# Optimization experiments

Measured on AMD Instinct MI355X. Metric: run time of the kernel, lower is better.

Reference implementation:

```python
import jax, jax.numpy as jnp
import numpy as np

N = 2048          # num agents / graph nodes
D = 128           # n_actor == n_map
ALPHA = 0.2       # GAT leakyrelu alpha
NEG = -1e9
X_IDX = [4, 9, 14, 19]   # actors_inter_cat time indices per LSTM step
E_IDX = [0, 4, 9, 14]    # graph_adjs time indices per LSTM step


def setup_inputs() -> dict:
    key = jax.random.key(0)
    ks = jax.random.split(key, 10)
    xavier = lambda k, shape: jax.random.uniform(
        k, shape, jnp.float32, -1.0, 1.0) * 1.414 * np.sqrt(6.0 / (shape[-2] + shape[-1]))
    actors_inter_cat = jax.random.normal(ks[0], (N, 20, D), jnp.float32)
    graph_adjs = jax.random.randint(ks[1], (N, 20, N), 0, 2, jnp.int32)
    # 4 GAT_SRF gates (forget, input, input_cell, output), stacked on leading axis
    Wg = xavier(ks[2], (4, 2 * D, D))          # gate projection W: in=2*D, out=D
    ag = xavier(ks[3], (4, 2 * D))             # attention vector a (2*out_features,)
    W = xavier(ks[4], (D, D))                  # GAT cell output projection
    b = xavier(ks[5], (1, D))
    h0 = xavier(ks[6], (1, D))
    conv_w = jax.random.normal(ks[7], (3, D, D, 2), jnp.float32) * (1.0 / np.sqrt(2 * D))
    conv_b = jax.random.normal(ks[8], (3, D), jnp.float32) * 0.01
    return {"actors_inter_cat": actors_inter_cat, "graph_adjs": graph_adjs,
            "Wg": Wg, "ag": ag, "W": W, "b": b, "h0": h0,
            "conv_w": conv_w, "conv_b": conv_b}


def _gat_gates(gin, mask, Wg, ag):
    # gin: (N, 2D); mask: (N, N) bool. Computes all 4 GAT_SRF gates at once.
    Wh = jnp.einsum('nf,gfo->gno', gin, Wg)                 # (4, N, D)
    s_src = jnp.einsum('gno,go->gn', Wh, ag[:, :D])         # a^T [Wh_i ..]
    s_dst = jnp.einsum('gno,go->gn', Wh, ag[:, D:])
    e = jax.nn.leaky_relu(s_src[:, :, None] + s_dst[:, None, :], ALPHA)  # (4,N,N)
    e = jnp.where(mask[None], e, NEG)
    attn = jax.nn.softmax(e, axis=-1)
    return jax.nn.elu(jnp.einsum('gnm,gmo->gno', attn, Wh))  # concat=True -> ELU


def reference(actors_inter_cat, graph_adjs, Wg, ag, W, b, h0, conv_w, conv_b):
    n = actors_inter_cat.shape[0]
    cell = actors_inter_cat[:, 0, :]
    hidden = jnp.broadcast_to(h0, (n, D))
    outs = []
    for t in range(4):  # fixed 4-step recurrence
        X = actors_inter_cat[:, X_IDX[t], :]
        mask = graph_adjs[:, E_IDX[t], :] > 0
        gin = jnp.concatenate([X, hidden], axis=1)          # (N, 2D)
        g = _gat_gates(gin, mask, Wg, ag)                   # (4, N, D)
        forget = jax.nn.sigmoid(g[0])
        inp_gate = jax.nn.sigmoid(g[1])
        inp_cell = jnp.tanh(g[2])
        out_gate = jax.nn.sigmoid(g[3])
        cell = cell * forget + inp_gate * inp_cell
        hidden = jnp.tanh(cell) * out_gate
        outs.append(jax.nn.sigmoid(hidden @ W + b))
    y = jnp.stack(outs, axis=2)                             # (N, D, 4)
    for l in range(3):  # kernel-2 Conv1d stack: length 4 -> 3 -> 2 -> 1
        y = (jnp.einsum('nct,oc->not', y[:, :, :-1], conv_w[l, :, :, 0])
             + jnp.einsum('nct,oc->not', y[:, :, 1:], conv_w[l, :, :, 1])
             + conv_b[l][None, :, None])
    return y[:, :, 0]                                       # squeeze -> (N, D)
```

## Files before the change

### kernel.cpp

```cpp
#include <hip/hip_runtime.h>

typedef __attribute__((ext_vector_type(8))) short short8;
typedef __attribute__((ext_vector_type(4))) float floatx4;

#define MFMA16(a,b,c) __builtin_amdgcn_mfma_f32_16x16x32_bf16(a,b,c,0,0,0)

__device__ __forceinline__ unsigned short f2bf(float f){
  unsigned u = __float_as_uint(f);
  u += 0x7fffu + ((u >> 16) & 1u);
  return (unsigned short)(u >> 16);
}
__device__ __forceinline__ float sigm(float x){ return 1.f/(1.f+__expf(-x)); }


__global__ __launch_bounds__(256) void prep_kernel(const float* __restrict__ actors,
    const float* __restrict__ Wg, const float* __restrict__ cw, const int* __restrict__ adj,
    float* __restrict__ cell, unsigned short* __restrict__ WgA, float* __restrict__ cwT,
    unsigned long long* __restrict__ bm){
  int bid = blockIdx.x;
  if (bid < 1024){
    int idx = bid*256 + threadIdx.x;
    int n = idx >> 7, c = idx & 127;
    cell[idx] = actors[(size_t)n*2560 + c];
  } else if (bid < 1536){
    int e = (bid-1024)*256 + threadIdx.x;
    int g = e >> 15, o = (e >> 8) & 127, k = e & 255;
    unsigned short v = f2bf(Wg[(size_t)g*32768 + k*128 + o]);
    int off = ((o>>4)*8 + (k>>5))*512 + (((k>>3)&3)*16 + (o&15))*8 + (k&7);
    WgA[(size_t)g*32768 + off] = v;
  } else if (bid < 1728){
    int e = (bid-1536)*256 + threadIdx.x;
    int l = e >> 14, rr = e & 16383, k = rr >> 7, o = rr & 127;
    cwT[(size_t)l*32768 + k*256 + o]       = cw[(size_t)l*32768 + o*256 + k*2];
    cwT[(size_t)l*32768 + k*256 + 128 + o] = cw[(size_t)l*32768 + o*256 + k*2 + 1];
  } else {
    const int E[4] = {0,4,9,14};
    int mb = bid - 1728;
    int t = mb & 3, nblk = mb >> 2;
    int wv = threadIdx.x >> 6, lane = threadIdx.x & 63;
    int n = nblk*4 + wv;
    const int* row = adj + (size_t)n*40960 + (size_t)E[t]*2048;
    unsigned long long* outp = bm + ((size_t)t*2048 + n)*32;
    for (int it=0; it<32; ++it){
      unsigned long long bal = __ballot(row[it*64 + lane] > 0);
      if (lane == 0) outp[it] = bal;
    }
  }
}

__global__ __launch_bounds__(512) void gatewh_kernel(const float* __restrict__ actors,
    const float* __restrict__ gbuf, float* __restrict__ cell, const float* __restrict__ h0,
    const float* __restrict__ W, const float* __restrict__ bvec,
    const unsigned short* __restrict__ WgA, const float* __restrict__ ag,
    float* __restrict__ y, unsigned short* __restrict__ WhB,
    float* __restrict__ spart, int xoff, int t){
  __shared__ float hl[16][132];
  __shared__ __align__(16) unsigned short ginb[16*264];
  __shared__ float sredS[4][4][16], sredD[4][4][16];
  int bx = blockIdx.x;
  int tile = bx >> 1, ohalf = bx & 1;
  int n0 = tile*16, tid = threadIdx.x;
  int row = tid>>5, q = tid&31;
  {
    int o0 = q*4;
    if (t == 0){
      *(float4*)&hl[row][o0] = *(const float4*)(h0 + o0);
    } else {
      size_t idx = (size_t)(n0+row)*128 + o0;
      float4 ga = *(const float4*)(gbuf+idx);
      float4 gb = *(const float4*)(gbuf+262144+idx);
      float4 gc = *(const float4*)(gbuf+524288+idx);
      float4 gd = *(const float4*)(gbuf+786432+idx);
      float4 cv = *(const float4*)(cell+idx);
      float fg[4]={ga.x,ga.y,ga.z,ga.w}, ig[4]={gb.x,gb.y,gb.z,gb.w};
      float ic[4]={gc.x,gc.y,gc.z,gc.w}, og[4]={gd.x,gd.y,gd.z,gd.w};
      float cc[4]={cv.x,cv.y,cv.z,cv.w};
      float clv[4];
      #pragma unroll
      for (int j=0;j<4;++j){
        clv[j] = cc[j]*sigm(fg[j]) + sigm(ig[j])*tanhf(ic[j]);
        hl[row][o0+j] = tanhf(clv[j])*sigm(og[j]);
      }
      if (ohalf == 0)
        *(float4*)(cell+idx) = (float4){clv[0],clv[1],clv[2],clv[3]};
    }
  }
  __syncthreads();
  if (t >= 1){
    int oc = ohalf*64 + q*2;
    float2 bb2 = *(const float2*)(bvec+oc);
    float a0 = bb2.x, a1 = bb2.y;
    const float* hr = hl[row];
    for (int k=0;k<128;++k){
      float hv = hr[k];
      float2 wv = *(const float2*)(W + (size_t)k*128 + oc);
      a0 += hv*wv.x; a1 += hv*wv.y;
    }
    float* yp = y + (size_t)(t-1)*262144 + (size_t)(n0+row)*128 + oc;
    yp[0] = sigm(a0); yp[1] = sigm(a1);
  }
  if (q < 16){
    const float* ap = actors + (size_t)(n0+row)*2560 + xoff + q*8;
    float4 a = *(const float4*)ap, bb = *(const float4*)(ap+4);
    unsigned short tmp[8] = {f2bf(a.x),f2bf(a.y),f2bf(a.z),f2bf(a.w),
                             f2bf(bb.x),f2bf(bb.y),f2bf(bb.z),f2bf(bb.w)};
    *(uint4*)&ginb[row*264 + q*8] = *(const uint4*)tmp;
  } else {
    int c0 = (q-16)*8;
    unsigned short tmp[8];
    #pragma unroll
    for (int j=0;j<8;++j) tmp[j] = f2bf(hl[row][c0+j]);
    *(uint4*)&ginb[row*264 + 128 + c0] = *(const uint4*)tmp;
  }
  __syncthreads();
  int w = tid>>6, lane = tid&63, quad = lane>>4, l16 = lane&15;
  int m32 = tile>>1, min32 = (tile&1)*16 + l16;
  int qp = min32>>3, jp = min32&7;
  #pragma unroll
  for (int ci=0; ci<2; ++ci){
    int cidx = w*2 + ci;
    int g = cidx>>2, o16q = cidx&3, o16 = ohalf*4 + o16q;
    floatx4 acc = {0.f,0.f,0.f,0.f};
    const unsigned short* wa = WgA + (size_t)g*32768;
    #pragma unroll
    for (int kh=0; kh<8; ++kh){
      short8 bfr = *(const short8*)&ginb[l16*264 + kh*32 + quad*8];
      short8 a0 = *(const short8*)(wa + (size_t)((o16*8 + kh)*64 + lane)*8);
      acc = MFMA16(a0, bfr, acc);
    }
    float ps = 0.f, pd = 0.f;
    unsigned short* wb = WhB + (size_t)(g*8 + o16)*32768 + m32*512 + qp*128 + jp;
    const float* agp = ag + g*256;
    #pragma unroll
    for (int r=0;r<4;++r){
      int o = o16*16 + quad*4 + r;
      float v = acc[r];
      ps += v*agp[o]; pd += v*agp[128+o];
      wb[(quad*4+r)*8] = f2bf(v);
    }
    ps += __shfl_down(ps,32); ps += __shfl_down(ps,16);
    pd += __shfl_down(pd,32); pd += __shfl_down(pd,16);
    if (lane < 16){ sredS[g][o16q][l16] = ps; sredD[g][o16q][l16] = pd; }
  }
  __syncthreads();
  if (tid < 128){
    int g = tid>>5, which = (tid>>4)&1, n = tid&15;
    float s;
    if (which) s = sredD[g][0][n]+sredD[g][1][n]+sredD[g][2][n]+sredD[g][3][n];
    else       s = sredS[g][0][n]+sredS[g][1][n]+sredS[g][2][n]+sredS[g][3][n];
    spart[(size_t)((ohalf*2 + which)*4 + g)*2048 + n0 + n] = s;
  }
}

__global__ __launch_bounds__(512) void attn_kernel(const unsigned char* __restrict__ bmb,
    const unsigned short* __restrict__ WhB, const float* __restrict__ spart,
    float* __restrict__ gout, int t){
  __shared__ float obuf[4][32][132];
  __shared__ float zpart[8][32];
  int g = blockIdx.y, n0 = blockIdx.x*32, tid = threadIdx.x;
  int w = tid>>6, lane = tid&63, quad = lane>>4, l16 = lane&15;
  const float* sS0 = spart + (size_t)(0 + g)*2048;
  const float* sD0 = spart + (size_t)(4 + g)*2048;
  const float* sS1 = spart + (size_t)(8 + g)*2048;
  const float* sD1 = spart + (size_t)(12 + g)*2048;
  float srcv0 = sS0[n0 + l16]      + sS1[n0 + l16];
  float srcv1 = sS0[n0 + 16 + l16] + sS1[n0 + 16 + l16];
  const unsigned char* mr0 = bmb + ((size_t)t*2048 + n0 + l16)*256 + w*32;
  const unsigned char* mr1 = mr0 + 16*256;
  uint4 q0 = *(const uint4*)mr0, q1 = *(const uint4*)(mr0+16);
  uint4 r0 = *(const uint4*)mr1, r1 = *(const uint4*)(mr1+16);
  unsigned mwd0[8] = {q0.x,q0.y,q0.z,q0.w, q1.x,q1.y,q1.z,q1.w};
  unsigned mwd1[8] = {r0.x,r0.y,r0.z,r0.w, r1.x,r1.y,r1.z,r1.w};
  const unsigned short* wb = WhB + (size_t)g*262144;
  float z0 = 0.f, z1 = 0.f;
  floatx4 acc0[8], acc1[8];
  #pragma unroll
  for (int j=0;j<8;++j){ acc0[j] = (floatx4){0.f,0.f,0.f,0.f}; acc1[j] = acc0[j]; }
  #pragma unroll
  for (int c=0; c<8; ++c){
    int mk = w*256 + c*32 + quad*8;
    float4 sa0 = *(const float4*)(sD0 + mk), sb0 = *(const float4*)(sD0 + mk + 4);
    float4 sa1 = *(const float4*)(sD1 + mk), sb1 = *(const float4*)(sD1 + mk + 4);
    unsigned mb0 = (mwd0[c] >> (quad*8)) & 0xffu;
    unsigned mb1 = (mwd1[c] >> (quad*8)) & 0xffu;
    float sv[8] = {sa0.x+sa1.x, sa0.y+sa1.y, sa0.z+sa1.z, sa0.w+sa1.w,
                   sb0.x+sb1.x, sb0.y+sb1.y, sb0.z+sb1.z, sb0.w+sb1.w};
    short8 A0, A1;
    #pragma unroll
    for (int j=0;j<8;++j){
      float s0 = srcv0 + sv[j];
      s0 = s0 > 0.f ? s0 : 0.2f*s0;
      float p0 = ((mb0 >> j) & 1u) ? __expf(s0) : 0.f;
      z0 += p0;
      A0[j] = (short)f2bf(p0);
      float s1 = srcv1 + sv[j];
      s1 = s1 > 0.f ? s1 : 0.2f*s1;
      float p1 = ((mb1 >> j) & 1u) ? __expf(s1) : 0.f;
      z1 += p1;
      A1[j] = (short)f2bf(p1);
    }
    const unsigned short* bp = wb + (size_t)(w*8 + c)*512 + lane*8;
    #pragma unroll
    for (int o16=0; o16<8; ++o16){
      short8 bfr = *(const short8*)(bp + (size_t)o16*32768);
      acc0[o16] = MFMA16(A0, bfr, acc0[o16]);
      acc1[o16] = MFMA16(A1, bfr, acc1[o16]);
    }
  }
  z0 += __shfl_down(z0,32); z0 += __shfl_down(z0,16);
  z1 += __shfl_down(z1,32); z1 += __shfl_down(z1,16);
  if (lane < 16){ zpart[w][l16] = z0; zpart[w][16+l16] = z1; }
  if (w < 4){
    #pragma unroll
    for (int o16=0;o16<8;++o16)
      #pragma unroll
      for (int r=0;r<4;++r){
        obuf[w][quad*4+r][o16*16+l16]      = acc0[o16][r];
        obuf[w][16+quad*4+r][o16*16+l16]   = acc1[o16][r];
      }
  }
  __syncthreads();
  if (w >= 4){
    #pragma unroll
    for (int o16=0;o16<8;++o16)
      #pragma unroll
      for (int r=0;r<4;++r){
        obuf[w-4][quad*4+r][o16*16+l16]    += acc0[o16][r];
        obuf[w-4][16+quad*4+r][o16*16+l16] += acc1[o16][r];
      }
  }
  __syncthreads();
  {
    int row = tid>>4, c0 = (tid&15)*8;
    float z = zpart[0][row]+zpart[1][row]+zpart[2][row]+zpart[3][row]
            + zpart[4][row]+zpart[5][row]+zpart[6][row]+zpart[7][row];
    float inv = 1.f / z;
    float* go = gout + (size_t)g*262144 + (size_t)(n0+row)*128 + c0;
    #pragma unroll
    for (int j=0;j<8;++j){
      float v = (obuf[0][row][c0+j] + obuf[1][row][c0+j]
               + obuf[2][row][c0+j] + obuf[3][row][c0+j]) * inv;
      go[j] = v > 0.f ? v : __expf(v) - 1.f;
    }
  }
}

__global__ __launch_bounds__(256) void convgate_kernel(const float* __restrict__ gbuf,
    const float* __restrict__ cell, const float* __restrict__ W, const float* __restrict__ bvec,
    const float* __restrict__ y, const float* __restrict__ cwT, const float* __restrict__ cb,
    float* __restrict__ out){
  __shared__ float hl[4][128];
  __shared__ float ylds[4][128][4];
  int tid = threadIdx.x;
  int r = tid >> 6, oc = (tid & 63)*2;
  int n = blockIdx.x*4 + r;
  size_t idx = (size_t)n*128 + oc;
  {
    float2 g0 = *(const float2*)(gbuf+idx),        g1 = *(const float2*)(gbuf+262144+idx);
    float2 g2 = *(const float2*)(gbuf+524288+idx), g3 = *(const float2*)(gbuf+786432+idx);
    float2 cv = *(const float2*)(cell+idx);
    float fg[2]={g0.x,g0.y}, ig[2]={g1.x,g1.y}, ic[2]={g2.x,g2.y}, og[2]={g3.x,g3.y};
    float cc[2]={cv.x,cv.y};
    #pragma unroll
    for (int j=0;j<2;++j){
      float cl = cc[j]*sigm(fg[j]) + sigm(ig[j])*tanhf(ic[j]);
      hl[r][oc+j] = tanhf(cl)*sigm(og[j]);
    }
  }
  {
    float2 y0 = *(const float2*)(y+idx), y1 = *(const float2*)(y+262144+idx),
           y2 = *(const float2*)(y+524288+idx);
    float a0[2]={y0.x,y0.y}, a1[2]={y1.x,y1.y}, a2[2]={y2.x,y2.y};
    #pragma unroll
    for (int j=0;j<2;++j){
      ylds[r][oc+j][0]=a0[j]; ylds[r][oc+j][1]=a1[j]; ylds[r][oc+j][2]=a2[j];
    }
  }
  __syncthreads();
  {
    float2 bb = *(const float2*)(bvec+oc);
    float acc[2] = {bb.x, bb.y};
    const float* hr = hl[r];
    for (int k=0;k<128;++k){
      float hv = hr[k];
      float2 wv = *(const float2*)(W + (size_t)k*128 + oc);
      acc[0]+=hv*wv.x; acc[1]+=hv*wv.y;
    }
    #pragma unroll
    for (int j=0;j<2;++j) ylds[r][oc+j][3] = sigm(acc[j]);
  }
  __syncthreads();
  {
    float a0[2]={0,0}, a1[2]={0,0}, a2[2]={0,0};
    for (int k=0;k<128;++k){
      float2 w0 = *(const float2*)(cwT + k*256 + oc);
      float2 w1 = *(const float2*)(cwT + k*256 + 128 + oc);
      float4 yv = *(const float4*)&ylds[r][k][0];
      float wa[2]={w0.x,w0.y}, wb2[2]={w1.x,w1.y};
      #pragma unroll
      for (int j=0;j<2;++j){
        a0[j] += yv.x*wa[j] + yv.y*wb2[j];
        a1[j] += yv.y*wa[j] + yv.z*wb2[j];
        a2[j] += yv.z*wa[j] + yv.w*wb2[j];
      }
    }
    float2 bb = *(const float2*)(cb+oc);
    float bbv[2]={bb.x,bb.y};
    __syncthreads();
    #pragma unroll
    for (int j=0;j<2;++j){
      ylds[r][oc+j][0]=a0[j]+bbv[j]; ylds[r][oc+j][1]=a1[j]+bbv[j]; ylds[r][oc+j][2]=a2[j]+bbv[j];
    }
    __syncthreads();
  }
  {
    float a0[2]={0,0}, a1[2]={0,0};
    for (int k=0;k<128;++k){
      float2 w0 = *(const float2*)(cwT + 32768 + k*256 + oc);
      float2 w1 = *(const float2*)(cwT + 32768 + k*256 + 128 + oc);
      float4 yv = *(const float4*)&ylds[r][k][0];
      float wa[2]={w0.x,w0.y}, wb2[2]={w1.x,w1.y};
      #pragma unroll
      for (int j=0;j<2;++j){
        a0[j] += yv.x*wa[j] + yv.y*wb2[j];
        a1[j] += yv.y*wa[j] + yv.z*wb2[j];
      }
    }
    float2 bb = *(const float2*)(cb+128+oc);
    float bbv[2]={bb.x,bb.y};
    __syncthreads();
    #pragma unroll
    for (int j=0;j<2;++j){
      ylds[r][oc+j][0]=a0[j]+bbv[j]; ylds[r][oc+j][1]=a1[j]+bbv[j];
    }
    __syncthreads();
  }
  {
    float a0[2]={0,0};
    for (int k=0;k<128;++k){
      float2 w0 = *(const float2*)(cwT + 65536 + k*256 + oc);
      float2 w1 = *(const float2*)(cwT + 65536 + k*256 + 128 + oc);
      float4 yv = *(const float4*)&ylds[r][k][0];
      a0[0] += yv.x*w0.x + yv.y*w1.x;
      a0[1] += yv.x*w0.y + yv.y*w1.y;
    }
    float2 bb = *(const float2*)(cb+256+oc);
    float2 res = {a0[0]+bb.x, a0[1]+bb.y};
    *(float2*)(out+idx) = res;
  }
}

extern "C" void kernel_launch(void* const* d_in, const int* in_sizes, int n_in,
                              void* d_out, int out_size, void* d_ws, size_t ws_size,
                              hipStream_t stream) {
  const float* actors = (const float*)d_in[0];
  const int*   adj    = (const int*)d_in[1];
  const float* Wg     = (const float*)d_in[2];
  const float* ag     = (const float*)d_in[3];
  const float* W      = (const float*)d_in[4];
  const float* b      = (const float*)d_in[5];
  const float* h0     = (const float*)d_in[6];
  const float* cw     = (const float*)d_in[7];
  const float* cb     = (const float*)d_in[8];
  float* out = (float*)d_out;

  char* ws = (char*)d_ws;
  unsigned long long* bm = (unsigned long long*)ws;
  float* cell          = (float*)(ws + (size_t)(2u<<20));
  unsigned short* WgA  = (unsigned short*)(ws + (size_t)(3u<<20));
  float* cwT           = (float*)(ws + (size_t)3407872);
  float* spart         = (float*)(ws + (size_t)3932160);
  unsigned short* WhB  = (unsigned short*)(ws + (size_t)(4u<<20));
  float* gbuf          = (float*)(ws + (size_t)(7u<<20));
  float* yplanes       = (float*)(ws + (size_t)(11u<<20));

  const int XI[4] = {4, 9, 14, 19};

  prep_kernel<<<3776, 256, 0, stream>>>(actors, Wg, cw, adj, cell, WgA, cwT, bm);
  for (int t=0; t<4; ++t){
    gatewh_kernel<<<256, 512, 0, stream>>>(actors, gbuf, cell, h0, W, b, WgA, ag,
                                           yplanes, WhB, spart, XI[t]*128, t);
    attn_kernel<<<dim3(64,4), 512, 0, stream>>>((const unsigned char*)bm, WhB,
                                                spart, gbuf, t);
  }
  convgate_kernel<<<512, 256, 0, stream>>>(gbuf, cell, W, b, yplanes, cwT, cb, out);
}
```

Measured before the change: 605.7 us.

## Fuse per-step gate and attention kernels into one persistent kernel with grid barriers

Replaces the eight alternating gatewh/attn launches with a single persistent 256-block kernel that loops over the four recurrence steps. Phases are separated by an atomic-counter grid barrier, and the counter is reset in prep_kernel. This removes seven kernel launch gaps and their tail effects. The cost is spin-waiting at each barrier, plus the requirement that all 256 blocks are co-resident (LDS use grows because both phases' shared buffers are now live in one kernel). The leaky-relu also becomes fmaxf.

Measured after the change: 916.9 us. 1.51x slower.

```diff
diff --git a/kernel.cpp b/kernel.cpp
--- a/kernel.cpp
+++ b/kernel.cpp
@@ -12,12 +12,24 @@
 }
 __device__ __forceinline__ float sigm(float x){ return 1.f/(1.f+__expf(-x)); }
 
+__device__ __forceinline__ void gridbar(unsigned* cnt, unsigned target){
+  __syncthreads();
+  if (threadIdx.x == 0){
+    __threadfence();
+    atomicAdd(cnt, 1u);
+    while (atomicAdd(cnt, 0u) < target) __builtin_amdgcn_s_sleep(1);
+    __threadfence();
+  }
+  __syncthreads();
+}
+
 
 __global__ __launch_bounds__(256) void prep_kernel(const float* __restrict__ actors,
     const float* __restrict__ Wg, const float* __restrict__ cw, const int* __restrict__ adj,
     float* __restrict__ cell, unsigned short* __restrict__ WgA, float* __restrict__ cwT,
-    unsigned long long* __restrict__ bm){
+    unsigned long long* __restrict__ bm, unsigned* __restrict__ barcnt){
   int bid = blockIdx.x;
+  if (bid == 0 && threadIdx.x == 0) barcnt[0] = 0u;
   if (bid < 1024){
     int idx = bid*256 + threadIdx.x;
     int n = idx >> 7, c = idx & 127;
@@ -48,200 +60,207 @@
   }
 }
 
-__global__ __launch_bounds__(512) void gatewh_kernel(const float* __restrict__ actors,
-    const float* __restrict__ gbuf, float* __restrict__ cell, const float* __restrict__ h0,
+__global__ __launch_bounds__(512) void fused_kernel(const float* __restrict__ actors,
+    float* __restrict__ gbuf, float* __restrict__ cell, const float* __restrict__ h0,
     const float* __restrict__ W, const float* __restrict__ bvec,
     const unsigned short* __restrict__ WgA, const float* __restrict__ ag,
     float* __restrict__ y, unsigned short* __restrict__ WhB,
-    float* __restrict__ spart, int xoff, int t){
+    float* __restrict__ spart, const unsigned char* __restrict__ bmb,
+    unsigned* __restrict__ barcnt){
   __shared__ float hl[16][132];
   __shared__ __align__(16) unsigned short ginb[16*264];
   __shared__ float sredS[4][4][16], sredD[4][4][16];
-  int bx = blockIdx.x;
-  int tile = bx >> 1, ohalf = bx & 1;
-  int n0 = tile*16, tid = threadIdx.x;
-  int row = tid>>5, q = tid&31;
-  {
-    int o0 = q*4;
-    if (t == 0){
-      *(float4*)&hl[row][o0] = *(const float4*)(h0 + o0);
-    } else {
-      size_t idx = (size_t)(n0+row)*128 + o0;
-      float4 ga = *(const float4*)(gbuf+idx);
-      float4 gb = *(const float4*)(gbuf+262144+idx);
-      float4 gc = *(const float4*)(gbuf+524288+idx);
-      float4 gd = *(const float4*)(gbuf+786432+idx);
-      float4 cv = *(const float4*)(cell+idx);
-      float fg[4]={ga.x,ga.y,ga.z,ga.w}, ig[4]={gb.x,gb.y,gb.z,gb.w};
-      float ic[4]={gc.x,gc.y,gc.z,gc.w}, og[4]={gd.x,gd.y,gd.z,gd.w};
-      float cc[4]={cv.x,cv.y,cv.z,cv.w};
-      float clv[4];
-      #pragma unroll
-      for (int j=0;j<4;++j){
-        clv[j] = cc[j]*sigm(fg[j]) + sigm(ig[j])*tanhf(ic[j]);
-        hl[row][o0+j] = tanhf(clv[j])*sigm(og[j]);
-      }
-      if (ohalf == 0)
-        *(float4*)(cell+idx) = (float4){clv[0],clv[1],clv[2],clv[3]};
-    }
-  }
-  __syncthreads();
-  if (t >= 1){
-    int oc = ohalf*64 + q*2;
-    float2 bb2 = *(const float2*)(bvec+oc);
-    float a0 = bb2.x, a1 = bb2.y;
-    const float* hr = hl[row];
-    for (int k=0;k<128;++k){
-      float hv = hr[k];
-      float2 wv = *(const float2*)(W + (size_t)k*128 + oc);
-      a0 += hv*wv.x; a1 += hv*wv.y;
-    }
-    float* yp = y + (size_t)(t-1)*262144 + (size_t)(n0+row)*128 + oc;
-    yp[0] = sigm(a0); yp[1] = sigm(a1);
-  }
-  if (q < 16){
-    const float* ap = actors + (size_t)(n0+row)*2560 + xoff + q*8;
-    float4 a = *(const float4*)ap, bb = *(const float4*)(ap+4);
-    unsigned short tmp[8] = {f2bf(a.x),f2bf(a.y),f2bf(a.z),f2bf(a.w),
-                             f2bf(bb.x),f2bf(bb.y),f2bf(bb.z),f2bf(bb.w)};
-    *(uint4*)&ginb[row*264 + q*8] = *(const uint4*)tmp;
-  } else {
-    int c0 = (q-16)*8;
-    unsigned short tmp[8];
-    #pragma unroll
-    for (int j=0;j<8;++j) tmp[j] = f2bf(hl[row][c0+j]);
-    *(uint4*)&ginb[row*264 + 128 + c0] = *(const uint4*)tmp;
-  }
-  __syncthreads();
-  int w = tid>>6, lane = tid&63, quad = lane>>4, l16 = lane&15;
-  int m32 = tile>>1, min32 = (tile&1)*16 + l16;
-  int qp = min32>>3, jp = min32&7;
-  #pragma unroll
-  for (int ci=0; ci<2; ++ci){
-    int cidx = w*2 + ci;
-    int g = cidx>>2, o16q = cidx&3, o16 = ohalf*4 + o16q;
-    floatx4 acc = {0.f,0.f,0.f,0.f};
-    const unsigned short* wa = WgA + (size_t)g*32768;
-    #pragma unroll
-    for (int kh=0; kh<8; ++kh){
-      short8 bfr = *(const short8*)&ginb[l16*264 + kh*32 + quad*8];
-      short8 a0 = *(const short8*)(wa + (size_t)((o16*8 + kh)*64 + lane)*8);
-      acc = MFMA16(a0, bfr, acc);
-    }
-    float ps = 0.f, pd = 0.f;
-    unsigned short* wb = WhB + (size_t)(g*8 + o16)*32768 + m32*512 + qp*128 + jp;
-    const float* agp = ag + g*256;
-    #pragma unroll
-    for (int r=0;r<4;++r){
-      int o = o16*16 + quad*4 + r;
-      float v = acc[r];
-      ps += v*agp[o]; pd += v*agp[128+o];
-      wb[(quad*4+r)*8] = f2bf(v);
-    }
-    ps += __shfl_down(ps,32); ps += __shfl_down(ps,16);
-    pd += __shfl_down(pd,32); pd += __shfl_down(pd,16);
-    if (lane < 16){ sredS[g][o16q][l16] = ps; sredD[g][o16q][l16] = pd; }
-  }
-  __syncthreads();
-  if (tid < 128){
-    int g = tid>>5, which = (tid>>4)&1, n = tid&15;
-    float s;
-    if (which) s = sredD[g][0][n]+sredD[g][1][n]+sredD[g][2][n]+sredD[g][3][n];
-    else       s = sredS[g][0][n]+sredS[g][1][n]+sredS[g][2][n]+sredS[g][3][n];
-    spart[(size_t)((ohalf*2 + which)*4 + g)*2048 + n0 + n] = s;
-  }
-}
-
-__global__ __launch_bounds__(512) void attn_kernel(const unsigned char* __restrict__ bmb,
-    const unsigned short* __restrict__ WhB, const float* __restrict__ spart,
-    float* __restrict__ gout, int t){
   __shared__ float obuf[4][32][132];
   __shared__ float zpart[8][32];
-  int g = blockIdx.y, n0 = blockIdx.x*32, tid = threadIdx.x;
-  int w = tid>>6, lane = tid&63, quad = lane>>4, l16 = lane&15;
-  const float* sS0 = spart + (size_t)(0 + g)*2048;
-  const float* sD0 = spart + (size_t)(4 + g)*2048;
-  const float* sS1 = spart + (size_t)(8 + g)*2048;
-  const float* sD1 = spart + (size_t)(12 + g)*2048;
-  float srcv0 = sS0[n0 + l16]      + sS1[n0 + l16];
-  float srcv1 = sS0[n0 + 16 + l16] + sS1[n0 + 16 + l16];
-  const unsigned char* mr0 = bmb + ((size_t)t*2048 + n0 + l16)*256 + w*32;
-  const unsigned char* mr1 = mr0 + 16*256;
-  uint4 q0 = *(const uint4*)mr0, q1 = *(const uint4*)(mr0+16);
-  uint4 r0 = *(const uint4*)mr1, r1 = *(const uint4*)(mr1+16);
-  unsigned mwd0[8] = {q0.x,q0.y,q0.z,q0.w, q1.x,q1.y,q1.z,q1.w};
-  unsigned mwd1[8] = {r0.x,r0.y,r0.z,r0.w, r1.x,r1.y,r1.z,r1.w};
-  const unsigned short* wb = WhB + (size_t)g*262144;
-  float z0 = 0.f, z1 = 0.f;
-  floatx4 acc0[8], acc1[8];
-  #pragma unroll
-  for (int j=0;j<8;++j){ acc0[j] = (floatx4){0.f,0.f,0.f,0.f}; acc1[j] = acc0[j]; }
-  #pragma unroll
-  for (int c=0; c<8; ++c){
-    int mk = w*256 + c*32 + quad*8;
-    float4 sa0 = *(const float4*)(sD0 + mk), sb0 = *(const float4*)(sD0 + mk + 4);
-    float4 sa1 = *(const float4*)(sD1 + mk), sb1 = *(const float4*)(sD1 + mk + 4);
-    unsigned mb0 = (mwd0[c] >> (quad*8)) & 0xffu;
-    unsigned mb1 = (mwd1[c] >> (quad*8)) & 0xffu;
-    float sv[8] = {sa0.x+sa1.x, sa0.y+sa1.y, sa0.z+sa1.z, sa0.w+sa1.w,
-                   sb0.x+sb1.x, sb0.y+sb1.y, sb0.z+sb1.z, sb0.w+sb1.w};
-    short8 A0, A1;
-    #pragma unroll
-    for (int j=0;j<8;++j){
-      float s0 = srcv0 + sv[j];
-      s0 = s0 > 0.f ? s0 : 0.2f*s0;
-      float p0 = ((mb0 >> j) & 1u) ? __expf(s0) : 0.f;
-      z0 += p0;
-      A0[j] = (short)f2bf(p0);
-      float s1 = srcv1 + sv[j];
-      s1 = s1 > 0.f ? s1 : 0.2f*s1;
-      float p1 = ((mb1 >> j) & 1u) ? __expf(s1) : 0.f;
-      z1 += p1;
-      A1[j] = (short)f2bf(p1);
-    }
-    const unsigned short* bp = wb + (size_t)(w*8 + c)*512 + lane*8;
-    #pragma unroll
-    for (int o16=0; o16<8; ++o16){
-      short8 bfr = *(const short8*)(bp + (size_t)o16*32768);
-      acc0[o16] = MFMA16(A0, bfr, acc0[o16]);
-      acc1[o16] = MFMA16(A1, bfr, acc1[o16]);
-    }
-  }
-  z0 += __shfl_down(z0,32); z0 += __shfl_down(z0,16);
-  z1 += __shfl_down(z1,32); z1 += __shfl_down(z1,16);
-  if (lane < 16){ zpart[w][l16] = z0; zpart[w][16+l16] = z1; }
-  if (w < 4){
-    #pragma unroll
-    for (int o16=0;o16<8;++o16)
+  int bid = blockIdx.x, tid = threadIdx.x;
+
+  #pragma unroll 1
+  for (int t=0; t<4; ++t){
+    int xoff = (t==0 ? 4 : t==1 ? 9 : t==2 ? 14 : 19) * 128;
+    {
+      int tile = bid >> 1, ohalf = bid & 1;
+      int n0 = tile*16;
+      int row = tid>>5, q = tid&31;
+      {
+        int o0 = q*4;
+        if (t == 0){
+          *(float4*)&hl[row][o0] = *(const float4*)(h0 + o0);
+        } else {
+          size_t idx = (size_t)(n0+row)*128 + o0;
+          float4 ga = *(const float4*)(gbuf+idx);
+          float4 gb = *(const float4*)(gbuf+262144+idx);
+          float4 gc = *(const float4*)(gbuf+524288+idx);
+          float4 gd = *(const float4*)(gbuf+786432+idx);
+          float4 cv = *(const float4*)(cell+idx);
+          float fg[4]={ga.x,ga.y,ga.z,ga.w}, ig[4]={gb.x,gb.y,gb.z,gb.w};
+          float ic[4]={gc.x,gc.y,gc.z,gc.w}, og[4]={gd.x,gd.y,gd.z,gd.w};
+          float cc[4]={cv.x,cv.y,cv.z,cv.w};
+          float clv[4];
+          #pragma unroll
+          for (int j=0;j<4;++j){
+            clv[j] = cc[j]*sigm(fg[j]) + sigm(ig[j])*tanhf(ic[j]);
+            hl[row][o0+j] = tanhf(clv[j])*sigm(og[j]);
+          }
+          if (ohalf == 0)
+            *(float4*)(cell+idx) = (float4){clv[0],clv[1],clv[2],clv[3]};
+        }
+      }
+      __syncthreads();
+      if (t >= 1){
+        int oc = ohalf*64 + q*2;
+        float2 bb2 = *(const float2*)(bvec+oc);
+        float a0 = bb2.x, a1 = bb2.y;
+        const float* hr = hl[row];
+        for (int k=0;k<128;++k){
+          float hv = hr[k];
+          float2 wv = *(const float2*)(W + (size_t)k*128 + oc);
+          a0 += hv*wv.x; a1 += hv*wv.y;
+        }
+        float* yp = y + (size_t)(t-1)*262144 + (size_t)(n0+row)*128 + oc;
+        yp[0] = sigm(a0); yp[1] = sigm(a1);
+      }
+      if (q < 16){
+        const float* ap = actors + (size_t)(n0+row)*2560 + xoff + q*8;
+        float4 a = *(const float4*)ap, bb = *(const float4*)(ap+4);
+        unsigned short tmp[8] = {f2bf(a.x),f2bf(a.y),f2bf(a.z),f2bf(a.w),
+                                 f2bf(bb.x),f2bf(bb.y),f2bf(bb.z),f2bf(bb.w)};
+        *(uint4*)&ginb[row*264 + q*8] = *(const uint4*)tmp;
+      } else {
+        int c0 = (q-16)*8;
+        unsigned short tmp[8];
+        #pragma unroll
+        for (int j=0;j<8;++j) tmp[j] = f2bf(hl[row][c0+j]);
+        *(uint4*)&ginb[row*264 + 128 + c0] = *(const uint4*)tmp;
+      }
+      __syncthreads();
+      int w = tid>>6, lane = tid&63, quad = lane>>4, l16 = lane&15;
+      int m32 = tile>>1, min32 = (tile&1)*16 + l16;
+      int qp = min32>>3, jp = min32&7;
       #pragma unroll
-      for (int r=0;r<4;++r){
-        obuf[w][quad*4+r][o16*16+l16]      = acc0[o16][r];
-        obuf[w][16+quad*4+r][o16*16+l16]   = acc1[o16][r];
-      }
-  }
-  __syncthreads();
-  if (w >= 4){
-    #pragma unroll
-    for (int o16=0;o16<8;++o16)
+      for (int ci=0; ci<2; ++ci){
+        int cidx = w*2 + ci;
+        int g = cidx>>2, o16q = cidx&3, o16 = ohalf*4 + o16q;
+        floatx4 acc = {0.f,0.f,0.f,0.f};
+        const unsigned short* wa = WgA + (size_t)g*32768;
+        #pragma unroll
+        for (int kh=0; kh<8; ++kh){
+          short8 bfr = *(const short8*)&ginb[l16*264 + kh*32 + quad*8];
+          short8 a0 = *(const short8*)(wa + (size_t)((o16*8 + kh)*64 + lane)*8);
+          acc = MFMA16(a0, bfr, acc);
+        }
+        float ps = 0.f, pd = 0.f;
+        unsigned short* wb = WhB + (size_t)(g*8 + o16)*32768 + m32*512 + qp*128 + jp;
+        const float* agp = ag + g*256;
+        #pragma unroll
+        for (int r=0;r<4;++r){
+          int o = o16*16 + quad*4 + r;
+          float v = acc[r];
+          ps += v*agp[o]; pd += v*agp[128+o];
+          wb[(quad*4+r)*8] = f2bf(v);
+        }
+        ps += __shfl_down(ps,32); ps += __shfl_down(ps,16);
+        pd += __shfl_down(pd,32); pd += __shfl_down(pd,16);
+        if (lane < 16){ sredS[g][o16q][l16] = ps; sredD[g][o16q][l16] = pd; }
+      }
+      __syncthreads();
+      if (tid < 128){
+        int g = tid>>5, which = (tid>>4)&1, n = tid&15;
+        float s;
+        if (which) s = sredD[g][0][n]+sredD[g][1][n]+sredD[g][2][n]+sredD[g][3][n];
+        else       s = sredS[g][0][n]+sredS[g][1][n]+sredS[g][2][n]+sredS[g][3][n];
+        spart[(size_t)((ohalf*2 + which)*4 + g)*2048 + n0 + n] = s;
+      }
+    }
+    gridbar(barcnt, (unsigned)(2*t+1)*256u);
+    {
+      int g = bid >> 6, n0 = (bid & 63)*32;
+      int w = tid>>6, lane = tid&63, quad = lane>>4, l16 = lane&15;
+      const float* sS0 = spart + (size_t)(0 + g)*2048;
+      const float* sD0 = spart + (size_t)(4 + g)*2048;
+      const float* sS1 = spart + (size_t)(8 + g)*2048;
+      const float* sD1 = spart + (size_t)(12 + g)*2048;
+      float srcv0 = sS0[n0 + l16]      + sS1[n0 + l16];
+      float srcv1 = sS0[n0 + 16 + l16] + sS1[n0 + 16 + l16];
+      const unsigned char* mr0 = bmb + ((size_t)t*2048 + n0 + l16)*256 + w*32;
+      const unsigned char* mr1 = mr0 + 16*256;
+      uint4 q0 = *(const uint4*)mr0, q1 = *(const uint4*)(mr0+16);
+      uint4 r0 = *(const uint4*)mr1, r1 = *(const uint4*)(mr1+16);
+      unsigned mwd0[8] = {q0.x,q0.y,q0.z,q0.w, q1.x,q1.y,q1.z,q1.w};
+      unsigned mwd1[8] = {r0.x,r0.y,r0.z,r0.w, r1.x,r1.y,r1.z,r1.w};
+      const unsigned short* wb = WhB + (size_t)g*262144;
+      float z0 = 0.f, z1 = 0.f;
+      floatx4 acc0[8], acc1[8];
       #pragma unroll
-      for (int r=0;r<4;++r){
-        obuf[w-4][quad*4+r][o16*16+l16]    += acc0[o16][r];
-        obuf[w-4][16+quad*4+r][o16*16+l16] += acc1[o16][r];
-      }
-  }
-  __syncthreads();
-  {
-    int row = tid>>4, c0 = (tid&15)*8;
-    float z = zpart[0][row]+zpart[1][row]+zpart[2][row]+zpart[3][row]
-            + zpart[4][row]+zpart[5][row]+zpart[6][row]+zpart[7][row];
-    float inv = 1.f / z;
-    float* go = gout + (size_t)g*262144 + (size_t)(n0+row)*128 + c0;
-    #pragma unroll
-    for (int j=0;j<8;++j){
-      float v = (obuf[0][row][c0+j] + obuf[1][row][c0+j]
-               + obuf[2][row][c0+j] + obuf[3][row][c0+j]) * inv;
-      go[j] = v > 0.f ? v : __expf(v) - 1.f;
-    }
+      for (int j=0;j<8;++j){ acc0[j] = (floatx4){0.f,0.f,0.f,0.f}; acc1[j] = acc0[j]; }
+      #pragma unroll
+      for (int c=0; c<8; ++c){
+        int mk = w*256 + c*32 + quad*8;
+        float4 sa0 = *(const float4*)(sD0 + mk), sb0 = *(const float4*)(sD0 + mk + 4);
+        float4 sa1 = *(const float4*)(sD1 + mk), sb1 = *(const float4*)(sD1 + mk + 4);
+        unsigned mb0 = (mwd0[c] >> (quad*8)) & 0xffu;
+        unsigned mb1 = (mwd1[c] >> (quad*8)) & 0xffu;
+        float sv[8] = {sa0.x+sa1.x, sa0.y+sa1.y, sa0.z+sa1.z, sa0.w+sa1.w,
+                       sb0.x+sb1.x, sb0.y+sb1.y, sb0.z+sb1.z, sb0.w+sb1.w};
+        short8 A0, A1;
+        #pragma unroll
+        for (int j=0;j<8;++j){
+          float s0 = srcv0 + sv[j];
+          s0 = fmaxf(s0, 0.2f*s0);
+          float p0 = ((mb0 >> j) & 1u) ? __expf(s0) : 0.f;
+          z0 += p0;
+          A0[j] = (short)f2bf(p0);
+          float s1 = srcv1 + sv[j];
+          s1 = fmaxf(s1, 0.2f*s1);
+          float p1 = ((mb1 >> j) & 1u) ? __expf(s1) : 0.f;
+          z1 += p1;
+          A1[j] = (short)f2bf(p1);
+        }
+        const unsigned short* bp = wb + (size_t)(w*8 + c)*512 + lane*8;
+        #pragma unroll
+        for (int o16=0; o16<8; ++o16){
+          short8 bfr = *(const short8*)(bp + (size_t)o16*32768);
+          acc0[o16] = MFMA16(A0, bfr, acc0[o16]);
+          acc1[o16] = MFMA16(A1, bfr, acc1[o16]);
+        }
+      }
+      z0 += __shfl_down(z0,32); z0 += __shfl_down(z0,16);
+      z1 += __shfl_down(z1,32); z1 += __shfl_down(z1,16);
+      if (lane < 16){ zpart[w][l16] = z0; zpart[w][16+l16] = z1; }
+      if (w < 4){
+        #pragma unroll
+        for (int o16=0;o16<8;++o16)
+          #pragma unroll
+          for (int r=0;r<4;++r){
+            obuf[w][quad*4+r][o16*16+l16]      = acc0[o16][r];
+            obuf[w][16+quad*4+r][o16*16+l16]   = acc1[o16][r];
+          }
+      }
+      __syncthreads();
+      if (w >= 4){
+        #pragma unroll
+        for (int o16=0;o16<8;++o16)
+          #pragma unroll
+          for (int r=0;r<4;++r){
+            obuf[w-4][quad*4+r][o16*16+l16]    += acc0[o16][r];
+            obuf[w-4][16+quad*4+r][o16*16+l16] += acc1[o16][r];
+          }
+      }
+      __syncthreads();
+      {
+        int row = tid>>4, c0 = (tid&15)*8;
+        float z = zpart[0][row]+zpart[1][row]+zpart[2][row]+zpart[3][row]
+                + zpart[4][row]+zpart[5][row]+zpart[6][row]+zpart[7][row];
+        float inv = 1.f / z;
+        float* go = gbuf + (size_t)g*262144 + (size_t)(n0+row)*128 + c0;
+        #pragma unroll
+        for (int j=0;j<8;++j){
+          float v = (obuf[0][row][c0+j] + obuf[1][row][c0+j]
+                   + obuf[2][row][c0+j] + obuf[3][row][c0+j]) * inv;
+          go[j] = v > 0.f ? v : __expf(v) - 1.f;
+        }
+      }
+    }
+    if (t < 3) gridbar(barcnt, (unsigned)(2*t+2)*256u);
   }
 }
 
@@ -373,15 +392,11 @@
   unsigned short* WhB  = (unsigned short*)(ws + (size_t)(4u<<20));
   float* gbuf          = (float*)(ws + (size_t)(7u<<20));
   float* yplanes       = (float*)(ws + (size_t)(11u<<20));
-
-  const int XI[4] = {4, 9, 14, 19};
-
-  prep_kernel<<<3776, 256, 0, stream>>>(actors, Wg, cw, adj, cell, WgA, cwT, bm);
-  for (int t=0; t<4; ++t){
-    gatewh_kernel<<<256, 512, 0, stream>>>(actors, gbuf, cell, h0, W, b, WgA, ag,
-                                           yplanes, WhB, spart, XI[t]*128, t);
-    attn_kernel<<<dim3(64,4), 512, 0, stream>>>((const unsigned char*)bm, WhB,
-                                                spart, gbuf, t);
-  }
+  unsigned* barcnt     = (unsigned*)(ws + (size_t)(14u<<20));
+
+  prep_kernel<<<3776, 256, 0, stream>>>(actors, Wg, cw, adj, cell, WgA, cwT, bm, barcnt);
+  fused_kernel<<<256, 512, 0, stream>>>(actors, gbuf, cell, h0, W, b, WgA, ag,
+                                        yplanes, WhB, spart, (const unsigned char*)bm,
+                                        barcnt);
   convgate_kernel<<<512, 256, 0, stream>>>(gbuf, cell, W, b, yplanes, cwT, cb, out);
 }
```
